# Kernel optimization log

Hardware: AMD Instinct MI355X
Metric: run time of the kernel (lower is better)

Reference implementation:

```python
import jax, jax.numpy as jnp
import numpy as np

B, N, L = 256, 4096, 6
EMBED, HID, VOCAB = 16, 32, 200
NOTE, LSTM_D, T = 64, 64, 128


def _tree_structure():
    """One random tree of N nodes (root=node 0), tiled across the batch.
    height = distance above deepest descendant; children have strictly smaller height."""
    rng = np.random.default_rng(0)
    height = np.zeros(N, np.int32)
    height[0] = L
    height[1:] = rng.integers(0, L, N - 1)
    kind = np.full(N, 2, np.int32)  # 2 = internal
    leaf_mask = height == 0
    kind[leaf_mask] = (rng.random(leaf_mask.sum()) < 0.1).astype(np.int32)  # 1=ptr, 0=leaf
    parent = np.zeros(N, np.int64)
    for hl in range(L):
        mask = height == hl
        cand = np.where((height > hl) & (kind == 2))[0]  # root always qualifies
        parent[mask] = rng.choice(cand, size=int(mask.sum()))
    parent[0] = 0  # root points to itself; harmless (its own h stays 0 until final level)
    return height, kind, parent


def setup_inputs():
    height, kind, parent = _tree_structure()
    offs = (np.arange(B, dtype=np.int64) * N)[:, None]
    rng = np.random.default_rng(1)
    inp = {
        'kind': jnp.asarray(np.tile(kind, B), jnp.int32),
        'height': jnp.asarray(np.tile(height, B), jnp.int32),
        'parent': jnp.asarray((parent[None, :] + offs).reshape(-1), jnp.int32),
        'tok_a': jnp.asarray(rng.integers(0, VOCAB, B * N), jnp.int32),
        'tok_b': jnp.asarray(rng.integers(0, VOCAB, B * N), jnp.int32),
        'ptr_time': jnp.asarray(rng.integers(0, T, B * N), jnp.int32),
    }
    key = jax.random.key(0)
    ks = jax.random.split(key, 16)
    def w(k, shape, scale=0.05):
        return (jax.random.normal(k, shape, jnp.float32) * scale)
    inp['first_notes'] = w(ks[0], (B, NOTE), 1.0)
    inp['lstm_out'] = w(ks[1], (B, T, LSTM_D), 1.0)
    inp['embedding'] = w(ks[2], (VOCAB, EMBED), 0.02)
    inp['leaf_w1'] = w(ks[3], (2 * EMBED, HID)); inp['leaf_b1'] = w(ks[4], (HID,))
    inp['leaf_w2'] = w(ks[5], (HID, HID));       inp['leaf_b2'] = w(ks[6], (HID,))
    inp['node_w'] = w(ks[7], (2 * EMBED + HID, HID)); inp['node_b'] = w(ks[8], (HID,))
    inp['ptr_w'] = w(ks[9], (NOTE + LSTM_D, HID));    inp['ptr_b'] = w(ks[10], (HID,))
    inp['ff_w1'] = w(ks[11], (HID, HID)); inp['ff_b1'] = w(ks[12], (HID,))
    inp['ff_w2'] = w(ks[13], (HID, HID)); inp['ff_b2'] = w(ks[14], (HID,))
    inp['tail_w'] = w(ks[15], (HID, 1)); inp['tail_b'] = jnp.zeros((1,), jnp.float32)
    return inp


def reference(kind, height, parent, tok_a, tok_b, ptr_time, first_notes, lstm_out,
              embedding, leaf_w1, leaf_b1, leaf_w2, leaf_b2, node_w, node_b,
              ptr_w, ptr_b, ff_w1, ff_b1, ff_w2, ff_b2, tail_w, tail_b):
    M = kind.shape[0]
    nb = first_notes.shape[0]
    n_per = M // nb
    tree_id = jnp.arange(M, dtype=jnp.int32) // n_per
    emb_a = embedding[tok_a]  # [M, EMBED] (parent-type / first-token embed)
    emb_b = embedding[tok_b]  # [M, EMBED] (node-type / second-token embed)
    pair = jnp.concatenate([emb_a, emb_b], axis=-1)  # [M, 2*EMBED]
    # leaf path: two stacked linears (no nonlinearity), as in leaf_ff
    leaf_h = (pair @ leaf_w1 + leaf_b1) @ leaf_w2 + leaf_b2
    # ptr path: Linear(note_dim + lstm_out_dim -> hidden)
    ptr_in = jnp.concatenate([first_notes[tree_id], lstm_out[tree_id, ptr_time]], axis=-1)
    ptr_h = ptr_in @ ptr_w + ptr_b
    h = jnp.where((kind == 0)[:, None], leaf_h,
                  jnp.where((kind == 1)[:, None], ptr_h, 0.0))
    # level-synchronous child-sum: children always have smaller height
    for lvl in range(1, L + 1):
        csum = jax.ops.segment_sum(h, parent, num_segments=M)  # [M, HID]
        inner = jax.nn.relu(jnp.concatenate([pair, csum], axis=-1) @ node_w + node_b)
        h = jnp.where((height == lvl)[:, None], inner, h)
    roots = h[::n_per]  # [B, HID], root is node 0 of each tree block
    ff = (roots @ ff_w1 + ff_b1) @ ff_w2 + ff_b2
    return ff @ tail_w + tail_b  # [B, 1]


if __name__ == '__main__':
    out = reference(**setup_inputs())
    print(out.shape, out.dtype)
```

## Files before the change

kernel.cpp:

```cpp
#include <hip/hip_runtime.h>

#define BATCH   256
#define N_PER   4096
#define EMBED   16
#define HID     32
#define NOTE    64
#define LSTM_D  64
#define T_LEN   128
#define VOCAB   200
#define HSTR    (BATCH * HID)

#define MH_C0    0
#define MH_C1    1
#define MH_CNT   2
#define MH_P     7
#define MH_PBASE 8
#define OFF_K0N   64
#define OFF_K1N   (OFF_K0N + N_PER)
#define OFF_PLIST (OFF_K1N + N_PER)
#define OFF_N2S   (OFF_PLIST + N_PER)
#define OFF_COFF  (OFF_N2S + N_PER)
#define EAW_BYTE     (1024 * 1024)
#define EBW_BYTE     (EAW_BYTE + 32 * 1024)
#define FNPRE_BYTE   (1536 * 1024)
#define PTRPRE_BYTE  (2ull * 1024 * 1024)
#define H_BYTE       (8ull * 1024 * 1024)

struct KParams {
    const int *kind, *height, *parent, *tok_a, *tok_b, *ptr_time;
    const float *first_notes, *lstm_out, *embedding;
    const float *leaf_w1, *leaf_b1, *leaf_w2, *leaf_b2;
    const float *node_w, *node_b, *ptr_w, *ptr_b;
    const float *ff_w1, *ff_b1, *ff_w2, *ff_b2, *tail_w, *tail_b;
    int *meta;
    float *eaw, *ebw, *fn_pre, *ptr_pre, *h, *out;
};

__global__ __launch_bounds__(1024) void prep_build_kernel(KParams p)
{
    __shared__ unsigned long long sp64[1024];
    __shared__ int spint[1024];
    __shared__ int sn2p[N_PER];
    __shared__ int sdeg[N_PER];
    __shared__ int sbases[8], stot[8];

    const int bid = blockIdx.x;
    const int t   = threadIdx.x;
    int* meta = p.meta;

    if (bid == 0) {
        const int i0 = 4 * t;
        int myb[4];
        unsigned long long clo = 0, chi = 0;
        #pragma unroll
        for (int q = 0; q < 4; ++q) {
            int i = i0 + q;
            int hgt = p.height[i];
            int b;
            if (hgt > 0) { b = 1 + hgt; if (b > 7) b = 7; }
            else b = (p.kind[i] == 0) ? 0 : 1;
            myb[q] = b;
            if (b < 4) clo += 1ull << (16 * b);
            else       chi += 1ull << (16 * (b - 4));
        }
        sp64[t] = clo; __syncthreads();
        for (int off = 1; off < 1024; off <<= 1) {
            unsigned long long v = (t >= off) ? sp64[t - off] : 0ull; __syncthreads();
            sp64[t] += v; __syncthreads();
        }
        unsigned long long ilo = sp64[t];
        if (t == 1023) {
            stot[0] = (int)(ilo & 0xFFFF);         stot[1] = (int)((ilo >> 16) & 0xFFFF);
            stot[2] = (int)((ilo >> 32) & 0xFFFF); stot[3] = (int)((ilo >> 48) & 0xFFFF);
        }
        __syncthreads();
        sp64[t] = chi; __syncthreads();
        for (int off = 1; off < 1024; off <<= 1) {
            unsigned long long v = (t >= off) ? sp64[t - off] : 0ull; __syncthreads();
            sp64[t] += v; __syncthreads();
        }
        unsigned long long ihi = sp64[t];
        if (t == 1023) {
            stot[4] = (int)(ihi & 0xFFFF);         stot[5] = (int)((ihi >> 16) & 0xFFFF);
            stot[6] = (int)((ihi >> 32) & 0xFFFF); stot[7] = (int)((ihi >> 48) & 0xFFFF);
        }
        __syncthreads();
        if (t == 0) {
            int s = 0;
            for (int b = 0; b < 8; ++b) { sbases[b] = s; s += stot[b]; }
            meta[MH_C0] = stot[0];
            meta[MH_C1] = stot[1];
            for (int l = 0; l < 5; ++l) meta[MH_CNT + l]   = stot[2 + l];
            for (int l = 0; l < 5; ++l) meta[MH_PBASE + l] = sbases[2 + l] - sbases[2];
            meta[MH_P] = (sbases[7] - sbases[2]) + stot[7];
        }
        __syncthreads();
        unsigned long long exlo = ilo - clo, exhi = ihi - chi;
        #pragma unroll
        for (int q = 0; q < 4; ++q) {
            int i = i0 + q, b = myb[q];
            int pos;
            if (b < 4) { pos = (int)((exlo >> (16 * b)) & 0xFFFF); exlo += 1ull << (16 * b); }
            else       { pos = (int)((exhi >> (16 * (b - 4))) & 0xFFFF); exhi += 1ull << (16 * (b - 4)); }
            if (b == 0)      meta[OFF_K0N + pos] = i;
            else if (b == 1) meta[OFF_K1N + pos] = i;
            else {
                int pidx = (sbases[b] - sbases[2]) + pos;
                meta[OFF_PLIST + pidx] = i;
                sn2p[i] = pidx;
            }
        }
        #pragma unroll
        for (int q = 0; q < 4; ++q) sdeg[i0 + q] = 0;
        __syncthreads();
        int par[4];
        #pragma unroll
        for (int q = 0; q < 4; ++q) {
            int i = i0 + q; par[q] = p.parent[i];
            if (i != 0) atomicAdd(&sdeg[sn2p[par[q]]], 1);
        }
        __syncthreads();
        int d0 = sdeg[i0], d1 = sdeg[i0 + 1], d2 = sdeg[i0 + 2], d3 = sdeg[i0 + 3];
        int s4 = d0 + d1 + d2 + d3;
        spint[t] = s4; __syncthreads();
        for (int off = 1; off < 1024; off <<= 1) {
            int v = (t >= off) ? spint[t - off] : 0; __syncthreads();
            spint[t] += v; __syncthreads();
        }
        int ex = spint[t] - s4;
        int o0 = ex, o1 = ex + d0, o2 = o1 + d1, o3 = o2 + d2;
        sdeg[i0] = o0; sdeg[i0 + 1] = o1; sdeg[i0 + 2] = o2; sdeg[i0 + 3] = o3;
        meta[OFF_COFF + i0]     = o0;
        meta[OFF_COFF + i0 + 1] = o1;
        meta[OFF_COFF + i0 + 2] = o2;
        meta[OFF_COFF + i0 + 3] = o3;
        if (t == 1023) meta[OFF_COFF + N_PER] = o3 + d3;
        __syncthreads();
        #pragma unroll
        for (int q = 0; q < 4; ++q) {
            int i = i0 + q;
            if (i != 0) {
                int slot = atomicAdd(&sdeg[sn2p[par[q]]], 1);
                meta[OFF_N2S + i] = slot;
            }
        }
    } else {
        int wt = (bid - 1) * 1024 + t;
        const int nw = 63 * 1024;
        int lane = t & 31;

        for (int idx = wt; idx < VOCAB * HID; idx += nw) {
            int v = idx >> 5, d = idx & 31;
            float sa = 0.f, sb = 0.f;
            #pragma unroll
            for (int k = 0; k < EMBED; ++k) {
                float e = p.embedding[v * EMBED + k];
                sa += e * p.node_w[k * HID + d];
                sb += e * p.node_w[(EMBED + k) * HID + d];
            }
            p.eaw[idx] = sa;
            p.ebw[idx] = sb;
        }
        {
            int wg = wt >> 5, nwg = nw >> 5;
            for (int r = wg; r < BATCH; r += nwg) {
                const float* fn = p.first_notes + (size_t)r * NOTE;
                float v = p.ptr_b[lane];
                #pragma unroll
                for (int k = 0; k < NOTE; ++k) v += fn[k] * p.ptr_w[k * HID + lane];
                p.fn_pre[r * HID + lane] = v;
            }
        }
        {
            int wave = wt >> 6, nwave = nw >> 6;
            int lane64 = wt & 63;
            for (int wb = wave; wb < (BATCH * T_LEN) / 64; wb += nwave) {
                int row = wb * 64 + lane64;
                const float4* lo4 = (const float4*)(p.lstm_out + (size_t)row * LSTM_D);
                float4 v0 = {0,0,0,0}, v1 = v0, v2 = v0, v3 = v0,
                       v4 = v0, v5 = v0, v6 = v0, v7 = v0;
                #pragma unroll
                for (int qq = 0; qq < 16; ++qq) {
                    float4 a = lo4[qq];
                    #define PMV(CK, KIDX) { \
                        const float4* wr = (const float4*)(p.ptr_w + (NOTE + (KIDX)) * HID); \
                        float4 w; \
                        w = wr[0]; v0.x += (CK)*w.x; v0.y += (CK)*w.y; v0.z += (CK)*w.z; v0.w += (CK)*w.w; \
                        w = wr[1]; v1.x += (CK)*w.x; v1.y += (CK)*w.y; v1.z += (CK)*w.z; v1.w += (CK)*w.w; \
                        w = wr[2]; v2.x += (CK)*w.x; v2.y += (CK)*w.y; v2.z += (CK)*w.z; v2.w += (CK)*w.w; \
                        w = wr[3]; v3.x += (CK)*w.x; v3.y += (CK)*w.y; v3.z += (CK)*w.z; v3.w += (CK)*w.w; \
                        w = wr[4]; v4.x += (CK)*w.x; v4.y += (CK)*w.y; v4.z += (CK)*w.z; v4.w += (CK)*w.w; \
                        w = wr[5]; v5.x += (CK)*w.x; v5.y += (CK)*w.y; v5.z += (CK)*w.z; v5.w += (CK)*w.w; \
                        w = wr[6]; v6.x += (CK)*w.x; v6.y += (CK)*w.y; v6.z += (CK)*w.z; v6.w += (CK)*w.w; \
                        w = wr[7]; v7.x += (CK)*w.x; v7.y += (CK)*w.y; v7.z += (CK)*w.z; v7.w += (CK)*w.w; }
                    PMV(a.x, 4 * qq + 0)
                    PMV(a.y, 4 * qq + 1)
                    PMV(a.z, 4 * qq + 2)
                    PMV(a.w, 4 * qq + 3)
                }
                float4* o = (float4*)(p.ptr_pre + (size_t)row * HID);
                o[0] = v0; o[1] = v1; o[2] = v2; o[3] = v3;
                o[4] = v4; o[5] = v5; o[6] = v6; o[7] = v7;
            }
        }
    }
}

__global__ __launch_bounds__(256, 4) void leafptr_kernel(KParams p)
{
    const int* meta = p.meta;
    const int* N2S  = meta + OFF_N2S;
    int lane = threadIdx.x & 31;
    int ggrp = (blockIdx.x * 256 + threadIdx.x) >> 5;
    int ngrp = (gridDim.x * 256) >> 5;

    int c0 = meta[MH_C0];
    const int* K0N = meta + OFF_K0N;
    float w1a[EMBED], w1b[EMBED], w2c[HID];
    #pragma unroll
    for (int k = 0; k < EMBED; ++k) {
        w1a[k] = p.leaf_w1[k * HID + lane];
        w1b[k] = p.leaf_w1[(EMBED + k) * HID + lane];
    }
    #pragma unroll
    for (int k = 0; k < HID; ++k) w2c[k] = p.leaf_w2[k * HID + lane];
    float b1 = p.leaf_b1[lane], b2 = p.leaf_b2[lane];

    int tot = c0 * BATCH;
    for (int i = ggrp; i < tot; i += ngrp) {
        int j = i >> 8, tree = i & 255;
        int node = K0N[j], slot = N2S[node];
        int gn = tree * N_PER + node;
        const float* ea = p.embedding + p.tok_a[gn] * EMBED;
        const float* eb = p.embedding + p.tok_b[gn] * EMBED;
        float hid = b1;
        #pragma unroll
        for (int k = 0; k < EMBED; ++k) hid += ea[k] * w1a[k];
        #pragma unroll
        for (int k = 0; k < EMBED; ++k) hid += eb[k] * w1b[k];
        float v = b2;
        #pragma unroll
        for (int k = 0; k < HID; ++k) v += __shfl(hid, k, 32) * w2c[k];
        p.h[(size_t)slot * HSTR + tree * HID + lane] = v;
    }

    int c1 = meta[MH_C1];
    const int* K1N = meta + OFF_K1N;
    int tot1 = c1 * BATCH;
    for (int i = ggrp; i < tot1; i += ngrp) {
        int j = i >> 8, tree = i & 255;
        int node = K1N[j], slot = N2S[node];
        int tt = p.ptr_time[tree * N_PER + node];
        float v = p.fn_pre[tree * HID + lane]
                + p.ptr_pre[((size_t)tree * T_LEN + tt) * HID + lane];
        p.h[(size_t)slot * HSTR + tree * HID + lane] = v;
    }
}

__global__ __launch_bounds__(256, 4) void level_kernel(KParams p, int l)
{
    const int* meta = p.meta;
    int cnt = meta[MH_CNT + l];
    int pb  = meta[MH_PBASE + l];
    const int* PL  = meta + OFF_PLIST;
    const int* N2S = meta + OFF_N2S;
    const int* CO  = meta + OFF_COFF;
    const float* W = p.node_w + 2 * EMBED * HID;

    int wave   = (blockIdx.x * 256 + threadIdx.x) >> 6;
    int nwave  = (gridDim.x * 256) >> 6;
    int lane64 = threadIdx.x & 63;

    int tot = cnt * 4;
    for (int i = wave; i < tot; i += nwave) {
        int rr = i >> 2, chunk = i & 3;
        int tree = chunk * 64 + lane64;
        int pidx = pb + rr;
        int node = PL[pidx], wslot = N2S[node];
        int e = CO[pidx], e1 = CO[pidx + 1];

        float4 c0 = {0,0,0,0}, c1 = c0, c2 = c0, c3 = c0,
               c4 = c0, c5 = c0, c6 = c0, c7 = c0;
        for (int c = e; c < e1; ++c) {
            const float4* row = (const float4*)(p.h + (size_t)c * HSTR + tree * HID);
            float4 x;
            x = row[0]; c0.x += x.x; c0.y += x.y; c0.z += x.z; c0.w += x.w;
            x = row[1]; c1.x += x.x; c1.y += x.y; c1.z += x.z; c1.w += x.w;
            x = row[2]; c2.x += x.x; c2.y += x.y; c2.z += x.z; c2.w += x.w;
            x = row[3]; c3.x += x.x; c3.y += x.y; c3.z += x.z; c3.w += x.w;
            x = row[4]; c4.x += x.x; c4.y += x.y; c4.z += x.z; c4.w += x.w;
            x = row[5]; c5.x += x.x; c5.y += x.y; c5.z += x.z; c5.w += x.w;
            x = row[6]; c6.x += x.x; c6.y += x.y; c6.z += x.z; c6.w += x.w;
            x = row[7]; c7.x += x.x; c7.y += x.y; c7.z += x.z; c7.w += x.w;
        }

        int gn = tree * N_PER + node;
        int ta = p.tok_a[gn], tb = p.tok_b[gn];
        const float4* A = (const float4*)(p.eaw + ta * HID);
        const float4* B = (const float4*)(p.ebw + tb * HID);
        const float4* NB = (const float4*)p.node_b;
        float4 v0, v1, v2, v3, v4, v5, v6, v7;
        #define INITV(VQ, Q) { float4 nb = NB[Q], a = A[Q], b = B[Q]; \
            VQ.x = nb.x + a.x + b.x; VQ.y = nb.y + a.y + b.y; \
            VQ.z = nb.z + a.z + b.z; VQ.w = nb.w + a.w + b.w; }
        INITV(v0,0) INITV(v1,1) INITV(v2,2) INITV(v3,3)
        INITV(v4,4) INITV(v5,5) INITV(v6,6) INITV(v7,7)

        #define MV(CK, KIDX) { \
            const float4* wr = (const float4*)(W + (KIDX) * HID); float4 w; \
            w = wr[0]; v0.x += (CK)*w.x; v0.y += (CK)*w.y; v0.z += (CK)*w.z; v0.w += (CK)*w.w; \
            w = wr[1]; v1.x += (CK)*w.x; v1.y += (CK)*w.y; v1.z += (CK)*w.z; v1.w += (CK)*w.w; \
            w = wr[2]; v2.x += (CK)*w.x; v2.y += (CK)*w.y; v2.z += (CK)*w.z; v2.w += (CK)*w.w; \
            w = wr[3]; v3.x += (CK)*w.x; v3.y += (CK)*w.y; v3.z += (CK)*w.z; v3.w += (CK)*w.w; \
            w = wr[4]; v4.x += (CK)*w.x; v4.y += (CK)*w.y; v4.z += (CK)*w.z; v4.w += (CK)*w.w; \
            w = wr[5]; v5.x += (CK)*w.x; v5.y += (CK)*w.y; v5.z += (CK)*w.z; v5.w += (CK)*w.w; \
            w = wr[6]; v6.x += (CK)*w.x; v6.y += (CK)*w.y; v6.z += (CK)*w.z; v6.w += (CK)*w.w; \
            w = wr[7]; v7.x += (CK)*w.x; v7.y += (CK)*w.y; v7.z += (CK)*w.z; v7.w += (CK)*w.w; }
        MV(c0.x, 0)  MV(c0.y, 1)  MV(c0.z, 2)  MV(c0.w, 3)
        MV(c1.x, 4)  MV(c1.y, 5)  MV(c1.z, 6)  MV(c1.w, 7)
        MV(c2.x, 8)  MV(c2.y, 9)  MV(c2.z, 10) MV(c2.w, 11)
        MV(c3.x, 12) MV(c3.y, 13) MV(c3.z, 14) MV(c3.w, 15)
        MV(c4.x, 16) MV(c4.y, 17) MV(c4.z, 18) MV(c4.w, 19)
        MV(c5.x, 20) MV(c5.y, 21) MV(c5.z, 22) MV(c5.w, 23)
        MV(c6.x, 24) MV(c6.y, 25) MV(c6.z, 26) MV(c6.w, 27)
        MV(c7.x, 28) MV(c7.y, 29) MV(c7.z, 30) MV(c7.w, 31)

        float4* o = (float4*)(p.h + (size_t)wslot * HSTR + tree * HID);
        #define STR(VQ, Q) { VQ.x = fmaxf(VQ.x, 0.f); VQ.y = fmaxf(VQ.y, 0.f); \
            VQ.z = fmaxf(VQ.z, 0.f); VQ.w = fmaxf(VQ.w, 0.f); o[Q] = VQ; }
        STR(v0,0) STR(v1,1) STR(v2,2) STR(v3,3)
        STR(v4,4) STR(v5,5) STR(v6,6) STR(v7,7)
    }
}

__global__ __launch_bounds__(256, 4) void root_final_kernel(KParams p)
{
    __shared__ float red[8][HID];
    const int* meta = p.meta;
    const int* CO = meta + OFF_COFF;
    int P = meta[MH_P];
    int e = CO[P - 1], e1 = CO[P];

    int tree = blockIdx.x;
    int grp  = threadIdx.x >> 5;
    int lane = threadIdx.x & 31;

    float part = 0.f;
    for (int c = e + grp; c < e1; c += 8)
        part += p.h[(size_t)c * HSTR + tree * HID + lane];
    red[grp][lane] = part;
    __syncthreads();

    if (grp == 0) {
        float csum = red[0][lane];
        #pragma unroll
        for (int g = 1; g < 8; ++g) csum += red[g][lane];

        int gn = tree * N_PER;
        int ta = p.tok_a[gn], tb = p.tok_b[gn];
        float v = p.node_b[lane] + p.eaw[ta * HID + lane] + p.ebw[tb * HID + lane];
        #pragma unroll
        for (int k = 0; k < HID; ++k)
            v += __shfl(csum, k, 32) * p.node_w[(2 * EMBED + k) * HID + lane];
        v = fmaxf(v, 0.f);

        float f1 = p.ff_b1[lane];
        #pragma unroll
        for (int k = 0; k < HID; ++k) f1 += __shfl(v, k, 32) * p.ff_w1[k * HID + lane];
        float f2 = p.ff_b2[lane];
        #pragma unroll
        for (int k = 0; k < HID; ++k) f2 += __shfl(f1, k, 32) * p.ff_w2[k * HID + lane];

        float c2 = f2 * p.tail_w[lane];
        #pragma unroll
        for (int off = 16; off > 0; off >>= 1) c2 += __shfl_down(c2, off, 32);
        if (lane == 0) p.out[tree] = c2 + p.tail_b[0];
    }
}

extern "C" void kernel_launch(void* const* d_in, const int* in_sizes, int n_in,
                              void* d_out, int out_size, void* d_ws, size_t ws_size,
                              hipStream_t stream) {
    char* ws = (char*)d_ws;
    KParams prm;
    prm.kind        = (const int*)d_in[0];
    prm.height      = (const int*)d_in[1];
    prm.parent      = (const int*)d_in[2];
    prm.tok_a       = (const int*)d_in[3];
    prm.tok_b       = (const int*)d_in[4];
    prm.ptr_time    = (const int*)d_in[5];
    prm.first_notes = (const float*)d_in[6];
    prm.lstm_out    = (const float*)d_in[7];
    prm.embedding   = (const float*)d_in[8];
    prm.leaf_w1     = (const float*)d_in[9];
    prm.leaf_b1     = (const float*)d_in[10];
    prm.leaf_w2     = (const float*)d_in[11];
    prm.leaf_b2     = (const float*)d_in[12];
    prm.node_w      = (const float*)d_in[13];
    prm.node_b      = (const float*)d_in[14];
    prm.ptr_w       = (const float*)d_in[15];
    prm.ptr_b       = (const float*)d_in[16];
    prm.ff_w1       = (const float*)d_in[17];
    prm.ff_b1       = (const float*)d_in[18];
    prm.ff_w2       = (const float*)d_in[19];
    prm.ff_b2       = (const float*)d_in[20];
    prm.tail_w      = (const float*)d_in[21];
    prm.tail_b      = (const float*)d_in[22];
    prm.meta     = (int*)ws;
    prm.eaw      = (float*)(ws + EAW_BYTE);
    prm.ebw      = (float*)(ws + EBW_BYTE);
    prm.fn_pre   = (float*)(ws + FNPRE_BYTE);
    prm.ptr_pre  = (float*)(ws + PTRPRE_BYTE);
    prm.h        = (float*)(ws + H_BYTE);
    prm.out      = (float*)d_out;

    prep_build_kernel<<<64, 1024, 0, stream>>>(prm);
    leafptr_kernel<<<1024, 256, 0, stream>>>(prm);
    for (int l = 0; l < 5; ++l)
        level_kernel<<<2048, 256, 0, stream>>>(prm, l);
    root_final_kernel<<<BATCH, 256, 0, stream>>>(prm);
}
```

Baseline: 492.9 us.

## Fold leaf MLP into per-token tables and index h by node with child lists

The two stacked leaf linears are folded into one 32x32 matrix. That matrix is applied to the embedding table to give per-token tables, so each leaf becomes two table lookups plus a bias. Nodes now store h at their node index, with a CSR child-index list instead of slot remapping. The prefix scans switch from shared-memory Hillis-Steele to wave shuffles, and grid sizes and launch bounds change. Child reads now go through one extra indirection and are scattered, so the contiguous-slot locality of the old layout is lost.

Measured after the change: 555.0 us. +12.6%, slower.

```diff
diff --git a/kernel.cpp b/kernel.cpp
--- a/kernel.cpp
+++ b/kernel.cpp
@@ -10,21 +10,19 @@
 #define VOCAB   200
 #define HSTR    (BATCH * HID)
 
-#define MH_C0    0
-#define MH_C1    1
-#define MH_CNT   2
-#define MH_P     7
-#define MH_PBASE 8
-#define OFF_K0N   64
-#define OFF_K1N   (OFF_K0N + N_PER)
-#define OFF_PLIST (OFF_K1N + N_PER)
-#define OFF_N2S   (OFF_PLIST + N_PER)
-#define OFF_COFF  (OFF_N2S + N_PER)
-#define EAW_BYTE     (1024 * 1024)
-#define EBW_BYTE     (EAW_BYTE + 32 * 1024)
-#define FNPRE_BYTE   (1536 * 1024)
-#define PTRPRE_BYTE  (2ull * 1024 * 1024)
-#define H_BYTE       (8ull * 1024 * 1024)
+#define MH_CNT   0
+#define MH_PBASE 5
+#define OFF_PLIST 64
+#define OFF_COFF  (OFF_PLIST + N_PER)
+#define OFF_CIDX  (OFF_COFF + N_PER + 1)
+#define EAW_BYTE    (1024 * 1024)
+#define EBW_BYTE    (EAW_BYTE + 32 * 1024)
+#define LEAFTA_BYTE (EAW_BYTE + 64 * 1024)
+#define LEAFTB_BYTE (EAW_BYTE + 96 * 1024)
+#define BF_BYTE     (EAW_BYTE + 128 * 1024)
+#define FNPRE_BYTE  (1536 * 1024)
+#define PTRPRE_BYTE (2ull * 1024 * 1024)
+#define H_BYTE      (8ull * 1024 * 1024)
 
 struct KParams {
     const int *kind, *height, *parent, *tok_a, *tok_b, *ptr_time;
@@ -33,239 +31,245 @@
     const float *node_w, *node_b, *ptr_w, *ptr_b;
     const float *ff_w1, *ff_b1, *ff_w2, *ff_b2, *tail_w, *tail_b;
     int *meta;
-    float *eaw, *ebw, *fn_pre, *ptr_pre, *h, *out;
+    float *eaw, *ebw, *leafTA, *leafTB, *bfused, *fn_pre, *ptr_pre, *h, *out;
 };
 
-__global__ __launch_bounds__(1024) void prep_build_kernel(KParams p)
+__global__ __launch_bounds__(1024) void k1_kernel(KParams p)
 {
-    __shared__ unsigned long long sp64[1024];
-    __shared__ int spint[1024];
-    __shared__ int sn2p[N_PER];
-    __shared__ int sdeg[N_PER];
-    __shared__ int sbases[8], stot[8];
-
     const int bid = blockIdx.x;
     const int t   = threadIdx.x;
-    int* meta = p.meta;
 
     if (bid == 0) {
-        const int i0 = 4 * t;
-        int myb[4];
-        unsigned long long clo = 0, chi = 0;
+        __shared__ unsigned long long wtot64[16];
+        __shared__ int wtoti[16];
+        __shared__ int sb[5];
+        __shared__ int sdeg[N_PER];
+
+        int lane = t & 63, wid = t >> 6;
+        int i0 = 4 * t;
+        int hgt[4], par[4];
+        unsigned long long cnt = 0;
         #pragma unroll
         for (int q = 0; q < 4; ++q) {
             int i = i0 + q;
-            int hgt = p.height[i];
-            int b;
-            if (hgt > 0) { b = 1 + hgt; if (b > 7) b = 7; }
-            else b = (p.kind[i] == 0) ? 0 : 1;
-            myb[q] = b;
-            if (b < 4) clo += 1ull << (16 * b);
-            else       chi += 1ull << (16 * (b - 4));
-        }
-        sp64[t] = clo; __syncthreads();
-        for (int off = 1; off < 1024; off <<= 1) {
-            unsigned long long v = (t >= off) ? sp64[t - off] : 0ull; __syncthreads();
-            sp64[t] += v; __syncthreads();
-        }
-        unsigned long long ilo = sp64[t];
-        if (t == 1023) {
-            stot[0] = (int)(ilo & 0xFFFF);         stot[1] = (int)((ilo >> 16) & 0xFFFF);
-            stot[2] = (int)((ilo >> 32) & 0xFFFF); stot[3] = (int)((ilo >> 48) & 0xFFFF);
-        }
-        __syncthreads();
-        sp64[t] = chi; __syncthreads();
-        for (int off = 1; off < 1024; off <<= 1) {
-            unsigned long long v = (t >= off) ? sp64[t - off] : 0ull; __syncthreads();
-            sp64[t] += v; __syncthreads();
-        }
-        unsigned long long ihi = sp64[t];
-        if (t == 1023) {
-            stot[4] = (int)(ihi & 0xFFFF);         stot[5] = (int)((ihi >> 16) & 0xFFFF);
-            stot[6] = (int)((ihi >> 32) & 0xFFFF); stot[7] = (int)((ihi >> 48) & 0xFFFF);
-        }
-        __syncthreads();
+            hgt[q] = p.height[i];
+            par[q] = p.parent[i];
+            if (hgt[q] >= 1 && hgt[q] <= 5) cnt += 1ull << (12 * (hgt[q] - 1));
+        }
+        unsigned long long inc = cnt;
+        #pragma unroll
+        for (int off = 1; off < 64; off <<= 1) {
+            unsigned long long v = __shfl_up(inc, off, 64);
+            if (lane >= off) inc += v;
+        }
+        if (lane == 63) wtot64[wid] = inc;
+        __syncthreads();
+        if (t < 16) {
+            unsigned long long x = wtot64[t];
+            #pragma unroll
+            for (int off = 1; off < 16; off <<= 1) {
+                unsigned long long v = __shfl_up(x, off, 64);
+                if (t >= off) x += v;
+            }
+            wtot64[t] = x;
+        }
+        __syncthreads();
+        unsigned long long tot = wtot64[15];
+        unsigned long long ex  = ((wid > 0) ? wtot64[wid - 1] : 0ull) + inc - cnt;
         if (t == 0) {
             int s = 0;
-            for (int b = 0; b < 8; ++b) { sbases[b] = s; s += stot[b]; }
-            meta[MH_C0] = stot[0];
-            meta[MH_C1] = stot[1];
-            for (int l = 0; l < 5; ++l) meta[MH_CNT + l]   = stot[2 + l];
-            for (int l = 0; l < 5; ++l) meta[MH_PBASE + l] = sbases[2 + l] - sbases[2];
-            meta[MH_P] = (sbases[7] - sbases[2]) + stot[7];
-        }
-        __syncthreads();
-        unsigned long long exlo = ilo - clo, exhi = ihi - chi;
+            for (int l = 0; l < 5; ++l) {
+                int c = (int)((tot >> (12 * l)) & 0xFFF);
+                p.meta[MH_CNT + l]   = c;
+                p.meta[MH_PBASE + l] = s;
+                sb[l] = s;
+                s += c;
+            }
+        }
+        __syncthreads();
         #pragma unroll
         for (int q = 0; q < 4; ++q) {
-            int i = i0 + q, b = myb[q];
-            int pos;
-            if (b < 4) { pos = (int)((exlo >> (16 * b)) & 0xFFFF); exlo += 1ull << (16 * b); }
-            else       { pos = (int)((exhi >> (16 * (b - 4))) & 0xFFFF); exhi += 1ull << (16 * (b - 4)); }
-            if (b == 0)      meta[OFF_K0N + pos] = i;
-            else if (b == 1) meta[OFF_K1N + pos] = i;
-            else {
-                int pidx = (sbases[b] - sbases[2]) + pos;
-                meta[OFF_PLIST + pidx] = i;
-                sn2p[i] = pidx;
+            int i = i0 + q, hv = hgt[q];
+            if (hv >= 1 && hv <= 5) {
+                int l = hv - 1;
+                int pos = (int)((ex >> (12 * l)) & 0xFFF);
+                ex += 1ull << (12 * l);
+                p.meta[OFF_PLIST + sb[l] + pos] = i;
             }
         }
         #pragma unroll
         for (int q = 0; q < 4; ++q) sdeg[i0 + q] = 0;
         __syncthreads();
-        int par[4];
         #pragma unroll
         for (int q = 0; q < 4; ++q) {
-            int i = i0 + q; par[q] = p.parent[i];
-            if (i != 0) atomicAdd(&sdeg[sn2p[par[q]]], 1);
+            int i = i0 + q;
+            if (i != 0) atomicAdd(&sdeg[par[q]], 1);
         }
         __syncthreads();
         int d0 = sdeg[i0], d1 = sdeg[i0 + 1], d2 = sdeg[i0 + 2], d3 = sdeg[i0 + 3];
         int s4 = d0 + d1 + d2 + d3;
-        spint[t] = s4; __syncthreads();
-        for (int off = 1; off < 1024; off <<= 1) {
-            int v = (t >= off) ? spint[t - off] : 0; __syncthreads();
-            spint[t] += v; __syncthreads();
-        }
-        int ex = spint[t] - s4;
-        int o0 = ex, o1 = ex + d0, o2 = o1 + d1, o3 = o2 + d2;
+        int inci = s4;
+        #pragma unroll
+        for (int off = 1; off < 64; off <<= 1) {
+            int v = __shfl_up(inci, off, 64);
+            if (lane >= off) inci += v;
+        }
+        if (lane == 63) wtoti[wid] = inci;
+        __syncthreads();
+        if (t < 16) {
+            int x = wtoti[t];
+            #pragma unroll
+            for (int off = 1; off < 16; off <<= 1) {
+                int v = __shfl_up(x, off, 64);
+                if (t >= off) x += v;
+            }
+            wtoti[t] = x;
+        }
+        __syncthreads();
+        int exi = ((wid > 0) ? wtoti[wid - 1] : 0) + inci - s4;
+        int o0 = exi, o1 = exi + d0, o2 = o1 + d1, o3 = o2 + d2;
+        p.meta[OFF_COFF + i0]     = o0;
+        p.meta[OFF_COFF + i0 + 1] = o1;
+        p.meta[OFF_COFF + i0 + 2] = o2;
+        p.meta[OFF_COFF + i0 + 3] = o3;
         sdeg[i0] = o0; sdeg[i0 + 1] = o1; sdeg[i0 + 2] = o2; sdeg[i0 + 3] = o3;
-        meta[OFF_COFF + i0]     = o0;
-        meta[OFF_COFF + i0 + 1] = o1;
-        meta[OFF_COFF + i0 + 2] = o2;
-        meta[OFF_COFF + i0 + 3] = o3;
-        if (t == 1023) meta[OFF_COFF + N_PER] = o3 + d3;
+        if (t == 1023) p.meta[OFF_COFF + N_PER] = o3 + d3;
         __syncthreads();
         #pragma unroll
         for (int q = 0; q < 4; ++q) {
             int i = i0 + q;
             if (i != 0) {
-                int slot = atomicAdd(&sdeg[sn2p[par[q]]], 1);
-                meta[OFF_N2S + i] = slot;
-            }
-        }
-    } else {
-        int wt = (bid - 1) * 1024 + t;
-        const int nw = 63 * 1024;
-        int lane = t & 31;
-
-        for (int idx = wt; idx < VOCAB * HID; idx += nw) {
+                int pos = atomicAdd(&sdeg[par[q]], 1);
+                p.meta[OFF_CIDX + pos] = i;
+            }
+        }
+    } else if (bid == 1) {
+        __shared__ float sWf[32 * 32];
+        {
+            int k = t >> 5, d = t & 31;
+            float s = 0.f;
+            #pragma unroll
+            for (int m = 0; m < 32; ++m)
+                s += p.leaf_w1[k * 32 + m] * p.leaf_w2[m * 32 + d];
+            sWf[t] = s;
+        }
+        if (t < 32) {
+            float s = p.leaf_b2[t];
+            #pragma unroll
+            for (int k = 0; k < 32; ++k) s += p.leaf_b1[k] * p.leaf_w2[k * 32 + t];
+            p.bfused[t] = s;
+        }
+        __syncthreads();
+        for (int idx = t; idx < VOCAB * HID; idx += 1024) {
             int v = idx >> 5, d = idx & 31;
-            float sa = 0.f, sb = 0.f;
+            float la = 0.f, lb = 0.f, sa = 0.f, sb2 = 0.f;
             #pragma unroll
             for (int k = 0; k < EMBED; ++k) {
                 float e = p.embedding[v * EMBED + k];
-                sa += e * p.node_w[k * HID + d];
-                sb += e * p.node_w[(EMBED + k) * HID + d];
-            }
-            p.eaw[idx] = sa;
-            p.ebw[idx] = sb;
-        }
-        {
-            int wg = wt >> 5, nwg = nw >> 5;
-            for (int r = wg; r < BATCH; r += nwg) {
-                const float* fn = p.first_notes + (size_t)r * NOTE;
-                float v = p.ptr_b[lane];
-                #pragma unroll
-                for (int k = 0; k < NOTE; ++k) v += fn[k] * p.ptr_w[k * HID + lane];
-                p.fn_pre[r * HID + lane] = v;
-            }
-        }
-        {
-            int wave = wt >> 6, nwave = nw >> 6;
-            int lane64 = wt & 63;
-            for (int wb = wave; wb < (BATCH * T_LEN) / 64; wb += nwave) {
-                int row = wb * 64 + lane64;
-                const float4* lo4 = (const float4*)(p.lstm_out + (size_t)row * LSTM_D);
-                float4 v0 = {0,0,0,0}, v1 = v0, v2 = v0, v3 = v0,
-                       v4 = v0, v5 = v0, v6 = v0, v7 = v0;
-                #pragma unroll
-                for (int qq = 0; qq < 16; ++qq) {
-                    float4 a = lo4[qq];
-                    #define PMV(CK, KIDX) { \
-                        const float4* wr = (const float4*)(p.ptr_w + (NOTE + (KIDX)) * HID); \
-                        float4 w; \
-                        w = wr[0]; v0.x += (CK)*w.x; v0.y += (CK)*w.y; v0.z += (CK)*w.z; v0.w += (CK)*w.w; \
-                        w = wr[1]; v1.x += (CK)*w.x; v1.y += (CK)*w.y; v1.z += (CK)*w.z; v1.w += (CK)*w.w; \
-                        w = wr[2]; v2.x += (CK)*w.x; v2.y += (CK)*w.y; v2.z += (CK)*w.z; v2.w += (CK)*w.w; \
-                        w = wr[3]; v3.x += (CK)*w.x; v3.y += (CK)*w.y; v3.z += (CK)*w.z; v3.w += (CK)*w.w; \
-                        w = wr[4]; v4.x += (CK)*w.x; v4.y += (CK)*w.y; v4.z += (CK)*w.z; v4.w += (CK)*w.w; \
-                        w = wr[5]; v5.x += (CK)*w.x; v5.y += (CK)*w.y; v5.z += (CK)*w.z; v5.w += (CK)*w.w; \
-                        w = wr[6]; v6.x += (CK)*w.x; v6.y += (CK)*w.y; v6.z += (CK)*w.z; v6.w += (CK)*w.w; \
-                        w = wr[7]; v7.x += (CK)*w.x; v7.y += (CK)*w.y; v7.z += (CK)*w.z; v7.w += (CK)*w.w; }
-                    PMV(a.x, 4 * qq + 0)
-                    PMV(a.y, 4 * qq + 1)
-                    PMV(a.z, 4 * qq + 2)
-                    PMV(a.w, 4 * qq + 3)
-                }
-                float4* o = (float4*)(p.ptr_pre + (size_t)row * HID);
-                o[0] = v0; o[1] = v1; o[2] = v2; o[3] = v3;
-                o[4] = v4; o[5] = v5; o[6] = v6; o[7] = v7;
-            }
+                la  += e * sWf[k * 32 + d];
+                lb  += e * sWf[(EMBED + k) * 32 + d];
+                sa  += e * p.node_w[k * HID + d];
+                sb2 += e * p.node_w[(EMBED + k) * HID + d];
+            }
+            p.leafTA[idx] = la;
+            p.leafTB[idx] = lb;
+            p.eaw[idx]    = sa;
+            p.ebw[idx]    = sb2;
+        }
+        for (int idx = t; idx < BATCH * HID; idx += 1024) {
+            int r = idx >> 5, d = idx & 31;
+            float s = p.ptr_b[d];
+            #pragma unroll
+            for (int k = 0; k < NOTE; ++k)
+                s += p.first_notes[r * NOTE + k] * p.ptr_w[k * HID + d];
+            p.fn_pre[idx] = s;
+        }
+    } else {
+        int lane = t & 63;
+        int gw = (bid - 2) * 16 + (t >> 6);
+        int nw = (gridDim.x - 2) * 16;
+        for (int wb = gw; wb < (BATCH * T_LEN) / 64; wb += nw) {
+            int row = wb * 64 + lane;
+            const float4* lo4 = (const float4*)(p.lstm_out + (size_t)row * LSTM_D);
+            float4 v0 = {0,0,0,0}, v1 = v0, v2 = v0, v3 = v0,
+                   v4 = v0, v5 = v0, v6 = v0, v7 = v0;
+            #pragma unroll
+            for (int qq = 0; qq < 16; ++qq) {
+                float4 a = lo4[qq];
+                #define PMV(CK, KIDX) { \
+                    const float4* wr = (const float4*)(p.ptr_w + (NOTE + (KIDX)) * HID); \
+                    float4 w; \
+                    w = wr[0]; v0.x += (CK)*w.x; v0.y += (CK)*w.y; v0.z += (CK)*w.z; v0.w += (CK)*w.w; \
+                    w = wr[1]; v1.x += (CK)*w.x; v1.y += (CK)*w.y; v1.z += (CK)*w.z; v1.w += (CK)*w.w; \
+                    w = wr[2]; v2.x += (CK)*w.x; v2.y += (CK)*w.y; v2.z += (CK)*w.z; v2.w += (CK)*w.w; \
+                    w = wr[3]; v3.x += (CK)*w.x; v3.y += (CK)*w.y; v3.z += (CK)*w.z; v3.w += (CK)*w.w; \
+                    w = wr[4]; v4.x += (CK)*w.x; v4.y += (CK)*w.y; v4.z += (CK)*w.z; v4.w += (CK)*w.w; \
+                    w = wr[5]; v5.x += (CK)*w.x; v5.y += (CK)*w.y; v5.z += (CK)*w.z; v5.w += (CK)*w.w; \
+                    w = wr[6]; v6.x += (CK)*w.x; v6.y += (CK)*w.y; v6.z += (CK)*w.z; v6.w += (CK)*w.w; \
+                    w = wr[7]; v7.x += (CK)*w.x; v7.y += (CK)*w.y; v7.z += (CK)*w.z; v7.w += (CK)*w.w; }
+                PMV(a.x, 4 * qq + 0)
+                PMV(a.y, 4 * qq + 1)
+                PMV(a.z, 4 * qq + 2)
+                PMV(a.w, 4 * qq + 3)
+            }
+            float4* o = (float4*)(p.ptr_pre + (size_t)row * HID);
+            o[0] = v0; o[1] = v1; o[2] = v2; o[3] = v3;
+            o[4] = v4; o[5] = v5; o[6] = v6; o[7] = v7;
         }
     }
 }
 
-__global__ __launch_bounds__(256, 4) void leafptr_kernel(KParams p)
+__global__ __launch_bounds__(256) void leafptr_kernel(KParams p)
 {
-    const int* meta = p.meta;
-    const int* N2S  = meta + OFF_N2S;
-    int lane = threadIdx.x & 31;
-    int ggrp = (blockIdx.x * 256 + threadIdx.x) >> 5;
-    int ngrp = (gridDim.x * 256) >> 5;
-
-    int c0 = meta[MH_C0];
-    const int* K0N = meta + OFF_K0N;
-    float w1a[EMBED], w1b[EMBED], w2c[HID];
-    #pragma unroll
-    for (int k = 0; k < EMBED; ++k) {
-        w1a[k] = p.leaf_w1[k * HID + lane];
-        w1b[k] = p.leaf_w1[(EMBED + k) * HID + lane];
-    }
-    #pragma unroll
-    for (int k = 0; k < HID; ++k) w2c[k] = p.leaf_w2[k * HID + lane];
-    float b1 = p.leaf_b1[lane], b2 = p.leaf_b2[lane];
-
-    int tot = c0 * BATCH;
-    for (int i = ggrp; i < tot; i += ngrp) {
-        int j = i >> 8, tree = i & 255;
-        int node = K0N[j], slot = N2S[node];
+    int wave  = (blockIdx.x * 256 + threadIdx.x) >> 6;
+    int nwave = (gridDim.x * 256) >> 6;
+    int lane  = threadIdx.x & 63;
+
+    int tot = N_PER * 4;
+    const float4* BF = (const float4*)p.bfused;
+    for (int i = wave; i < tot; i += nwave) {
+        int node = i >> 2, chunk = i & 3;
+        if (p.height[node] != 0) continue;
+        int tree = chunk * 64 + lane;
         int gn = tree * N_PER + node;
-        const float* ea = p.embedding + p.tok_a[gn] * EMBED;
-        const float* eb = p.embedding + p.tok_b[gn] * EMBED;
-        float hid = b1;
-        #pragma unroll
-        for (int k = 0; k < EMBED; ++k) hid += ea[k] * w1a[k];
-        #pragma unroll
-        for (int k = 0; k < EMBED; ++k) hid += eb[k] * w1b[k];
-        float v = b2;
-        #pragma unroll
-        for (int k = 0; k < HID; ++k) v += __shfl(hid, k, 32) * w2c[k];
-        p.h[(size_t)slot * HSTR + tree * HID + lane] = v;
-    }
-
-    int c1 = meta[MH_C1];
-    const int* K1N = meta + OFF_K1N;
-    int tot1 = c1 * BATCH;
-    for (int i = ggrp; i < tot1; i += ngrp) {
-        int j = i >> 8, tree = i & 255;
-        int node = K1N[j], slot = N2S[node];
-        int tt = p.ptr_time[tree * N_PER + node];
-        float v = p.fn_pre[tree * HID + lane]
-                + p.ptr_pre[((size_t)tree * T_LEN + tt) * HID + lane];
-        p.h[(size_t)slot * HSTR + tree * HID + lane] = v;
+        float4* o = (float4*)(p.h + (size_t)node * HSTR + tree * HID);
+        if (p.kind[node] == 0) {
+            int ta = p.tok_a[gn], tb = p.tok_b[gn];
+            const float4* A = (const float4*)(p.leafTA + ta * HID);
+            const float4* B = (const float4*)(p.leafTB + tb * HID);
+            #pragma unroll
+            for (int q = 0; q < 8; ++q) {
+                float4 a = A[q], b = B[q], c = BF[q];
+                float4 r;
+                r.x = a.x + b.x + c.x; r.y = a.y + b.y + c.y;
+                r.z = a.z + b.z + c.z; r.w = a.w + b.w + c.w;
+                o[q] = r;
+            }
+        } else {
+            int tt = p.ptr_time[gn];
+            const float4* F = (const float4*)(p.fn_pre + tree * HID);
+            const float4* Q = (const float4*)(p.ptr_pre + ((size_t)tree * T_LEN + tt) * HID);
+            #pragma unroll
+            for (int q = 0; q < 8; ++q) {
+                float4 f = F[q], g = Q[q];
+                float4 r;
+                r.x = f.x + g.x; r.y = f.y + g.y;
+                r.z = f.z + g.z; r.w = f.w + g.w;
+                o[q] = r;
+            }
+        }
     }
 }
 
-__global__ __launch_bounds__(256, 4) void level_kernel(KParams p, int l)
+__global__ __launch_bounds__(256) void level_kernel(KParams p, int l)
 {
     const int* meta = p.meta;
     int cnt = meta[MH_CNT + l];
     int pb  = meta[MH_PBASE + l];
-    const int* PL  = meta + OFF_PLIST;
-    const int* N2S = meta + OFF_N2S;
-    const int* CO  = meta + OFF_COFF;
-    const float* W = p.node_w + 2 * EMBED * HID;
+    const int* PL   = meta + OFF_PLIST;
+    const int* CO   = meta + OFF_COFF;
+    const int* CIDX = meta + OFF_CIDX;
+    const float* W  = p.node_w + 2 * EMBED * HID;
 
     int wave   = (blockIdx.x * 256 + threadIdx.x) >> 6;
     int nwave  = (gridDim.x * 256) >> 6;
@@ -275,14 +279,14 @@
     for (int i = wave; i < tot; i += nwave) {
         int rr = i >> 2, chunk = i & 3;
         int tree = chunk * 64 + lane64;
-        int pidx = pb + rr;
-        int node = PL[pidx], wslot = N2S[node];
-        int e = CO[pidx], e1 = CO[pidx + 1];
+        int node = PL[pb + rr];
+        int e = CO[node], e1 = CO[node + 1];
 
         float4 c0 = {0,0,0,0}, c1 = c0, c2 = c0, c3 = c0,
                c4 = c0, c5 = c0, c6 = c0, c7 = c0;
         for (int c = e; c < e1; ++c) {
-            const float4* row = (const float4*)(p.h + (size_t)c * HSTR + tree * HID);
+            int cn = CIDX[c];
+            const float4* row = (const float4*)(p.h + (size_t)cn * HSTR + tree * HID);
             float4 x;
             x = row[0]; c0.x += x.x; c0.y += x.y; c0.z += x.z; c0.w += x.w;
             x = row[1]; c1.x += x.x; c1.y += x.y; c1.z += x.z; c1.w += x.w;
@@ -296,8 +300,8 @@
 
         int gn = tree * N_PER + node;
         int ta = p.tok_a[gn], tb = p.tok_b[gn];
-        const float4* A = (const float4*)(p.eaw + ta * HID);
-        const float4* B = (const float4*)(p.ebw + tb * HID);
+        const float4* A  = (const float4*)(p.eaw + ta * HID);
+        const float4* B  = (const float4*)(p.ebw + tb * HID);
         const float4* NB = (const float4*)p.node_b;
         float4 v0, v1, v2, v3, v4, v5, v6, v7;
         #define INITV(VQ, Q) { float4 nb = NB[Q], a = A[Q], b = B[Q]; \
@@ -325,7 +329,7 @@
         MV(c6.x, 24) MV(c6.y, 25) MV(c6.z, 26) MV(c6.w, 27)
         MV(c7.x, 28) MV(c7.y, 29) MV(c7.z, 30) MV(c7.w, 31)
 
-        float4* o = (float4*)(p.h + (size_t)wslot * HSTR + tree * HID);
+        float4* o = (float4*)(p.h + (size_t)node * HSTR + tree * HID);
         #define STR(VQ, Q) { VQ.x = fmaxf(VQ.x, 0.f); VQ.y = fmaxf(VQ.y, 0.f); \
             VQ.z = fmaxf(VQ.z, 0.f); VQ.w = fmaxf(VQ.w, 0.f); o[Q] = VQ; }
         STR(v0,0) STR(v1,1) STR(v2,2) STR(v3,3)
@@ -333,13 +337,12 @@
     }
 }
 
-__global__ __launch_bounds__(256, 4) void root_final_kernel(KParams p)
+__global__ __launch_bounds__(256) void root_final_kernel(KParams p)
 {
     __shared__ float red[8][HID];
-    const int* meta = p.meta;
-    const int* CO = meta + OFF_COFF;
-    int P = meta[MH_P];
-    int e = CO[P - 1], e1 = CO[P];
+    const int* CO   = p.meta + OFF_COFF;
+    const int* CIDX = p.meta + OFF_CIDX;
+    int e = CO[0], e1 = CO[1];
 
     int tree = blockIdx.x;
     int grp  = threadIdx.x >> 5;
@@ -347,7 +350,7 @@
 
     float part = 0.f;
     for (int c = e + grp; c < e1; c += 8)
-        part += p.h[(size_t)c * HSTR + tree * HID + lane];
+        part += p.h[(size_t)CIDX[c] * HSTR + tree * HID + lane];
     red[grp][lane] = part;
     __syncthreads();
 
@@ -406,17 +409,20 @@
     prm.ff_b2       = (const float*)d_in[20];
     prm.tail_w      = (const float*)d_in[21];
     prm.tail_b      = (const float*)d_in[22];
-    prm.meta     = (int*)ws;
-    prm.eaw      = (float*)(ws + EAW_BYTE);
-    prm.ebw      = (float*)(ws + EBW_BYTE);
-    prm.fn_pre   = (float*)(ws + FNPRE_BYTE);
-    prm.ptr_pre  = (float*)(ws + PTRPRE_BYTE);
-    prm.h        = (float*)(ws + H_BYTE);
-    prm.out      = (float*)d_out;
-
-    prep_build_kernel<<<64, 1024, 0, stream>>>(prm);
-    leafptr_kernel<<<1024, 256, 0, stream>>>(prm);
+    prm.meta    = (int*)ws;
+    prm.eaw     = (float*)(ws + EAW_BYTE);
+    prm.ebw     = (float*)(ws + EBW_BYTE);
+    prm.leafTA  = (float*)(ws + LEAFTA_BYTE);
+    prm.leafTB  = (float*)(ws + LEAFTB_BYTE);
+    prm.bfused  = (float*)(ws + BF_BYTE);
+    prm.fn_pre  = (float*)(ws + FNPRE_BYTE);
+    prm.ptr_pre = (float*)(ws + PTRPRE_BYTE);
+    prm.h       = (float*)(ws + H_BYTE);
+    prm.out     = (float*)d_out;
+
+    k1_kernel<<<64, 1024, 0, stream>>>(prm);
+    leafptr_kernel<<<512, 256, 0, stream>>>(prm);
     for (int l = 0; l < 5; ++l)
-        level_kernel<<<2048, 256, 0, stream>>>(prm, l);
+        level_kernel<<<1024, 256, 0, stream>>>(prm, l);
     root_final_kernel<<<BATCH, 256, 0, stream>>>(prm);
 }
```
